# Kernel optimization log

Measured on AMD Instinct MI355X. Metric: run time of the kernel, lower is better.

## Reference

```python
import jax, jax.numpy as jnp
import numpy as np

N_USER = 60000
N_ITEM = 120000
N = N_USER + N_ITEM
EMB = 64
LAYERS = [64, 64, 64]
BATCH = 4096
NNZ_ADJ = 3_600_000
NNZ_UG = 960_000
NNZ_IG = 1_920_000


def spmm(rows, cols, vals, x, n_rows):
    # sparse (COO) @ dense: out[r] += v * x[c]
    return jax.ops.segment_sum(vals[:, None] * x[cols], rows, num_segments=n_rows)


def l2_normalize(x, eps=1e-12):
    n = jnp.linalg.norm(x, axis=1, keepdims=True)
    return x / jnp.maximum(n, eps)


def setup_inputs() -> dict:
    key = jax.random.key(0)
    ks = jax.random.split(key, 24)
    s = 0.1  # xavier-like init scale for 64-dim fan
    inp = {
        'users': jax.random.randint(ks[0], (BATCH,), 0, N_USER),
        'pos_items': jax.random.randint(ks[1], (BATCH,), 0, N_ITEM),
        'neg_items': jax.random.randint(ks[2], (BATCH,), 0, N_ITEM),
        # normalized bipartite adjacency (COO)
        'adj_rows': jax.random.randint(ks[3], (NNZ_ADJ,), 0, N),
        'adj_cols': jax.random.randint(ks[4], (NNZ_ADJ,), 0, N),
        'adj_vals': jax.random.uniform(ks[5], (NNZ_ADJ,), jnp.float32) * 0.05,
        # user-user graph for user_GNN
        'ug_rows': jax.random.randint(ks[6], (NNZ_UG,), 0, N_USER),
        'ug_cols': jax.random.randint(ks[7], (NNZ_UG,), 0, N_USER),
        'ug_vals': jax.random.uniform(ks[8], (NNZ_UG,), jnp.float32) * 0.06,
        # item-item graph for item_GNN
        'ig_rows': jax.random.randint(ks[9], (NNZ_IG,), 0, N_ITEM),
        'ig_cols': jax.random.randint(ks[10], (NNZ_IG,), 0, N_ITEM),
        'ig_vals': jax.random.uniform(ks[11], (NNZ_IG,), jnp.float32) * 0.06,
        'user_emb': jax.random.normal(ks[12], (N_USER, EMB), jnp.float32) * s,
        'item_emb': jax.random.normal(ks[13], (N_ITEM, EMB), jnp.float32) * s,
        # NGCF propagation weights, stacked over 3 layers (all 64x64)
        'W_gc': jax.random.normal(ks[14], (3, EMB, EMB), jnp.float32) * s,
        'b_gc': jax.random.normal(ks[15], (3, 1, EMB), jnp.float32) * s,
        'W_bi': jax.random.normal(ks[16], (3, EMB, EMB), jnp.float32) * s,
        'b_bi': jax.random.normal(ks[17], (3, 1, EMB), jnp.float32) * s,
        # 2-layer GCN weights for user/item side graphs
        'Wu0': jax.random.normal(ks[18], (EMB, 64), jnp.float32) * s,
        'bu0': jnp.zeros((64,), jnp.float32),
        'Wu1': jax.random.normal(ks[19], (64, 64), jnp.float32) * s,
        'bu1': jnp.zeros((64,), jnp.float32),
        'Wi0': jax.random.normal(ks[20], (EMB, 64), jnp.float32) * s,
        'bi0': jnp.zeros((64,), jnp.float32),
        'Wi1': jax.random.normal(ks[21], (64, 64), jnp.float32) * s,
        'bi1': jnp.zeros((64,), jnp.float32),
    }
    return inp


def reference(users, pos_items, neg_items,
              adj_rows, adj_cols, adj_vals,
              ug_rows, ug_cols, ug_vals,
              ig_rows, ig_cols, ig_vals,
              user_emb, item_emb,
              W_gc, b_gc, W_bi, b_bi,
              Wu0, bu0, Wu1, bu1, Wi0, bi0, Wi1, bi1):
    # side GCNs on user-user / item-item graphs (2 GraphConv layers, elu between)
    u_h = jax.nn.elu(spmm(ug_rows, ug_cols, ug_vals, user_emb, N_USER) @ Wu0 + bu0)
    u_h = spmm(ug_rows, ug_cols, ug_vals, u_h, N_USER) @ Wu1 + bu1
    i_h = jax.nn.elu(spmm(ig_rows, ig_cols, ig_vals, item_emb, N_ITEM) @ Wi0 + bi0)
    i_h = spmm(ig_rows, ig_cols, ig_vals, i_h, N_ITEM) @ Wi1 + bi1

    # NGCF propagation on the bipartite graph
    ego = jnp.concatenate([user_emb, item_emb], axis=0)  # [N, 64]
    all_emb = [ego]
    for k in range(len(LAYERS)):
        side = spmm(adj_rows, adj_cols, adj_vals, ego, N)         # [N, 64]
        sum_e = side @ W_gc[k] + b_gc[k]
        bi_e = (ego * side) @ W_bi[k] + b_bi[k]
        ego = jax.nn.leaky_relu(sum_e + bi_e, negative_slope=0.2)
        all_emb.append(l2_normalize(ego))
    all_emb = jnp.concatenate(all_emb, axis=1)  # [N, 256]

    u_g = all_emb[:N_USER]
    i_g = all_emb[N_USER:]

    # in-place relu in the torch code mutates the GNN outputs before concat
    user_full = jnp.concatenate([u_g, jax.nn.relu(u_h)], axis=1)  # [N_USER, 320]
    item_full = jnp.concatenate([i_g, jax.nn.relu(i_h)], axis=1)  # [N_ITEM, 320]

    return (user_full[users], item_full[pos_items], item_full[neg_items])
```

## Files before the change

kernel.cpp:

```cpp
#include <hip/hip_runtime.h>
#include <hip/hip_bf16.h>

#define N_USER 60000
#define N_ITEM 120000
#define NTOT   180000
#define NNZ_ADJ 3600000
#define NNZ_UG   960000
#define NNZ_IG  1920000

#define RSB     2048
#define NSB_ADJ ((NTOT  + RSB - 1) / RSB)
#define NSB_UG  ((N_USER+ RSB - 1) / RSB)
#define NSB_IG  ((N_ITEM+ RSB - 1) / RSB)
#define CAPA_SB 43008
#define CAPU_SB 34816
#define CAPI_SB 34816
#define CHUNK   4096
#define PB_U ((NNZ_UG  + CHUNK - 1) / CHUNK)
#define PB_I ((NNZ_IG  + CHUNK - 1) / CHUNK)
#define PB_A ((NNZ_ADJ + CHUNK - 1) / CHUNK)

typedef __hip_bfloat16 bf16;
typedef __attribute__((ext_vector_type(8))) short bf16x8;
typedef __attribute__((ext_vector_type(4))) float f32x4;

__device__ __forceinline__ float ldf(const void* p, long i, int f) {
    return f ? ((const float*)p)[i] : __bfloat162float(((const bf16*)p)[i]);
}

__device__ __forceinline__ unsigned pk2(float a, float b) {
    unsigned short lo = __bfloat16_as_ushort(__float2bfloat16(a));
    unsigned short hi = __bfloat16_as_ushort(__float2bfloat16(b));
    return (unsigned)lo | ((unsigned)hi << 16);
}

__device__ __forceinline__ bf16x8 mul_bf8(bf16x8 x, bf16x8 y) {
    bf16x8 r;
#pragma unroll
    for (int e = 0; e < 8; e++) {
        float xf = __uint_as_float(((unsigned)(unsigned short)x[e]) << 16);
        float yf = __uint_as_float(((unsigned)(unsigned short)y[e]) << 16);
        r[e] = (short)__bfloat16_as_ushort(__float2bfloat16(xf * yf));
    }
    return r;
}

__global__ void k_detect(const void* __restrict__ vals, int* __restrict__ flag) {
    if (threadIdx.x == 0 && blockIdx.x == 0) {
        const unsigned short* w = (const unsigned short*)vals;
        int cnt = 0;
        for (int i = 0; i < 512; i += 2) cnt += (w[i] >> 15) & 1;
        *flag = (cnt > 16) ? 1 : 0;
    }
}

__global__ __launch_bounds__(256) void k_cast16(const void* __restrict__ ue,
                                                const void* __restrict__ ie,
                                                bf16* __restrict__ ego16,
                                                const int* __restrict__ flag) {
    int f = *flag;
    long i = (long)blockIdx.x * 256 + threadIdx.x;
    const long uN = (long)N_USER * 64;
    if (i < (long)NTOT * 64) {
        float v = (i < uN) ? ldf(ue, i, f) : ldf(ie, i - uN, f);
        ego16[i] = __float2bfloat16(v);
    }
}

__global__ void k_initpos3(int* __restrict__ sbU, int* __restrict__ sbI,
                           int* __restrict__ sbA) {
    int i = threadIdx.x;
    if (i < NSB_UG)  sbU[i * 16] = i * CAPU_SB;
    if (i < NSB_IG)  sbI[i * 16] = i * CAPI_SB;
    if (i < NSB_ADJ) sbA[i * 16] = i * CAPA_SB;
}

__global__ __launch_bounds__(256) void k_part3(const int* __restrict__ rU, const int* __restrict__ cU, const void* __restrict__ vU,
                                               const int* __restrict__ rI, const int* __restrict__ cI, const void* __restrict__ vI,
                                               const int* __restrict__ rA, const int* __restrict__ cA, const void* __restrict__ vA,
                                               uint2* __restrict__ recU, uint2* __restrict__ recI, uint2* __restrict__ recA,
                                               int* __restrict__ sbU, int* __restrict__ sbI, int* __restrict__ sbA,
                                               const int* __restrict__ flag) {
    __shared__ int lcnt[96];
    __shared__ int lstart[96];
    __shared__ int lpos[96];
    __shared__ int lbase[96];
    __shared__ int wtmp;
    __shared__ uint2 stage[CHUNK];
    __shared__ unsigned char sbin[CHUNK];

    int f = *flag;
    int t = threadIdx.x;
    int b = blockIdx.x;
    const int *rows, *cols; const void* vals; uint2* rec; int* sbpos; int nnz, base;
    if (b < PB_U)             { rows = rU; cols = cU; vals = vU; rec = recU; sbpos = sbU; nnz = NNZ_UG;  base = b * CHUNK; }
    else if (b < PB_U + PB_I) { rows = rI; cols = cI; vals = vI; rec = recI; sbpos = sbI; nnz = NNZ_IG;  base = (b - PB_U) * CHUNK; }
    else                      { rows = rA; cols = cA; vals = vA; rec = recA; sbpos = sbA; nnz = NNZ_ADJ; base = (b - PB_U - PB_I) * CHUNK; }

    if (t < 96) lcnt[t] = 0;

    int base16 = base + t * 16;
    int rr[16], cc[16];
    float vv[16];
    if (base + CHUNK <= nnz) {
#pragma unroll
        for (int k = 0; k < 4; k++) {
            int4 r4 = *(const int4*)(rows + base16 + 4 * k);
            int4 c4 = *(const int4*)(cols + base16 + 4 * k);
            rr[4 * k + 0] = r4.x; rr[4 * k + 1] = r4.y; rr[4 * k + 2] = r4.z; rr[4 * k + 3] = r4.w;
            cc[4 * k + 0] = c4.x; cc[4 * k + 1] = c4.y; cc[4 * k + 2] = c4.z; cc[4 * k + 3] = c4.w;
        }
        if (f) {
#pragma unroll
            for (int k = 0; k < 4; k++) {
                float4 v4 = *(const float4*)((const float*)vals + base16 + 4 * k);
                vv[4 * k + 0] = v4.x; vv[4 * k + 1] = v4.y; vv[4 * k + 2] = v4.z; vv[4 * k + 3] = v4.w;
            }
        } else {
            const unsigned short* vb = (const unsigned short*)vals;
#pragma unroll
            for (int h = 0; h < 2; h++) {
                uint4 q = *(const uint4*)(vb + base16 + 8 * h);
                vv[8 * h + 0] = __uint_as_float(q.x << 16);
                vv[8 * h + 1] = __uint_as_float(q.x & 0xFFFF0000u);
                vv[8 * h + 2] = __uint_as_float(q.y << 16);
                vv[8 * h + 3] = __uint_as_float(q.y & 0xFFFF0000u);
                vv[8 * h + 4] = __uint_as_float(q.z << 16);
                vv[8 * h + 5] = __uint_as_float(q.z & 0xFFFF0000u);
                vv[8 * h + 6] = __uint_as_float(q.w << 16);
                vv[8 * h + 7] = __uint_as_float(q.w & 0xFFFF0000u);
            }
        }
    } else {
#pragma unroll
        for (int k = 0; k < 16; k++) {
            int e = base16 + k;
            if (e < nnz) { rr[k] = rows[e]; cc[k] = cols[e]; vv[k] = ldf(vals, e, f); }
            else         { rr[k] = -1; cc[k] = 0; vv[k] = 0.0f; }
        }
    }
    __syncthreads();

#pragma unroll
    for (int k = 0; k < 16; k++)
        if (rr[k] >= 0) atomicAdd(&lcnt[rr[k] >> 11], 1);
    __syncthreads();

    int v = (t < 96) ? lcnt[t] : 0;
    int incl = v;
    {
        int lane = t & 63;
#pragma unroll
        for (int d = 1; d < 64; d <<= 1) {
            int w = __shfl_up(incl, d, 64);
            if (lane >= d) incl += w;
        }
    }
    if (t == 63) wtmp = incl;
    __syncthreads();
    if (t >= 64 && t < 96) incl += wtmp;
    if (t < 96) {
        int ex = incl - v;
        lstart[t] = ex;
        lpos[t]   = ex;
        lbase[t]  = v ? atomicAdd(&sbpos[t * 16], v) : 0;
    }
    __syncthreads();

#pragma unroll
    for (int k = 0; k < 16; k++) {
        if (rr[k] >= 0) {
            int sb = rr[k] >> 11;
            int o = atomicAdd(&lpos[sb], 1);
            stage[o] = make_uint2(((unsigned)(rr[k] & 2047) << 18) | (unsigned)cc[k],
                                  __float_as_uint(vv[k]));
            sbin[o] = (unsigned char)sb;
        }
    }
    __syncthreads();

    int total = lstart[95] + lcnt[95];
    for (int i = t; i < total; i += 256) {
        int sb = sbin[i];
        rec[lbase[sb] + (i - lstart[sb])] = stage[i];
    }
}

__global__ __launch_bounds__(1024) void k_sortsb3(
        const uint2* __restrict__ recU, uint2* __restrict__ rec2U, int* __restrict__ rstartU, int* __restrict__ rendU, const int* __restrict__ sbU,
        const uint2* __restrict__ recI, uint2* __restrict__ rec2I, int* __restrict__ rstartI, int* __restrict__ rendI, const int* __restrict__ sbI,
        const uint2* __restrict__ recA, uint2* __restrict__ rec2A, int* __restrict__ rstartA, int* __restrict__ rendA, const int* __restrict__ sbA) {
    __shared__ int cnt[RSB];
    __shared__ int pos[RSB];
    __shared__ int wsum[16];
    int b = blockIdx.x, t = threadIdx.x;
    const uint2* rec; uint2* rec2; int* rstart; int* rend; const int* sbpos;
    int cap, n_rows, lb;
    if (b < NSB_UG) {
        lb = b; rec = recU; rec2 = rec2U; rstart = rstartU; rend = rendU;
        sbpos = sbU; cap = CAPU_SB; n_rows = N_USER;
    } else if (b < NSB_UG + NSB_IG) {
        lb = b - NSB_UG; rec = recI; rec2 = rec2I; rstart = rstartI; rend = rendI;
        sbpos = sbI; cap = CAPI_SB; n_rows = N_ITEM;
    } else {
        lb = b - NSB_UG - NSB_IG; rec = recA; rec2 = rec2A; rstart = rstartA; rend = rendA;
        sbpos = sbA; cap = CAPA_SB; n_rows = NTOT;
    }
    int s = lb * cap;
    int e = sbpos[lb * 16];
    cnt[t] = 0; cnt[t + 1024] = 0;
    __syncthreads();
    int j = s + t;
    for (; j + 3072 < e; j += 4096) {
        uint2 r0 = rec[j];
        uint2 r1 = rec[j + 1024];
        uint2 r2 = rec[j + 2048];
        uint2 r3 = rec[j + 3072];
        atomicAdd(&cnt[r0.x >> 18], 1);
        atomicAdd(&cnt[r1.x >> 18], 1);
        atomicAdd(&cnt[r2.x >> 18], 1);
        atomicAdd(&cnt[r3.x >> 18], 1);
    }
    for (; j < e; j += 1024)
        atomicAdd(&cnt[rec[j].x >> 18], 1);
    __syncthreads();
    int a  = cnt[2 * t];
    int bb = cnt[2 * t + 1];
    int ps = a + bb;
    int incl = ps;
    int lane = t & 63;
#pragma unroll
    for (int d = 1; d < 64; d <<= 1) {
        int v = __shfl_up(incl, d, 64);
        if (lane >= d) incl += v;
    }
    int wv = t >> 6;
    if (lane == 63) wsum[wv] = incl;
    __syncthreads();
    if (t < 16) {
        int v  = wsum[t];
        int iv = v;
#pragma unroll
        for (int d = 1; d < 16; d <<= 1) {
            int w = __shfl_up(iv, d, 64);
            if (t >= d) iv += w;
        }
        wsum[t] = iv - v;
    }
    __syncthreads();
    int ex0 = wsum[wv] + (incl - ps);
    pos[2 * t]     = ex0;
    pos[2 * t + 1] = ex0 + a;
    int row0 = lb * RSB;
    {
        int ra = row0 + 2 * t;
        if (ra < n_rows) { rstart[ra] = s + ex0;      rend[ra] = s + ex0 + a; }
        int rb = ra + 1;
        if (rb < n_rows) { rstart[rb] = s + ex0 + a;  rend[rb] = s + ex0 + a + bb; }
    }
    __syncthreads();
    j = s + t;
    for (; j + 3072 < e; j += 4096) {
        uint2 r0 = rec[j];
        uint2 r1 = rec[j + 1024];
        uint2 r2 = rec[j + 2048];
        uint2 r3 = rec[j + 3072];
        int o0 = atomicAdd(&pos[r0.x >> 18], 1);
        int o1 = atomicAdd(&pos[r1.x >> 18], 1);
        int o2 = atomicAdd(&pos[r2.x >> 18], 1);
        int o3 = atomicAdd(&pos[r3.x >> 18], 1);
        rec2[s + o0] = r0;
        rec2[s + o1] = r1;
        rec2[s + o2] = r2;
        rec2[s + o3] = r3;
    }
    for (; j < e; j += 1024) {
        uint2 r = rec[j];
        int o = atomicAdd(&pos[r.x >> 18], 1);
        rec2[s + o] = r;
    }
}

#define ACC8(q, v)                                      \
    a[0] += (v) * __uint_as_float((q).x << 16);         \
    a[1] += (v) * __uint_as_float((q).x & 0xFFFF0000u); \
    a[2] += (v) * __uint_as_float((q).y << 16);         \
    a[3] += (v) * __uint_as_float((q).y & 0xFFFF0000u); \
    a[4] += (v) * __uint_as_float((q).z << 16);         \
    a[5] += (v) * __uint_as_float((q).z & 0xFFFF0000u); \
    a[6] += (v) * __uint_as_float((q).w << 16);         \
    a[7] += (v) * __uint_as_float((q).w & 0xFFFF0000u);

__device__ __forceinline__ void spmm_row(int row, int p,
                                         const int* __restrict__ rstart,
                                         const int* __restrict__ rend,
                                         const uint2* __restrict__ rec,
                                         const bf16* __restrict__ x,
                                         bf16* __restrict__ out) {
    int s = rstart[row], e = rend[row];
    const uint4* xb = (const uint4*)x;
    float a[8];
#pragma unroll
    for (int i = 0; i < 8; i++) a[i] = 0.0f;

    int j = s;
    for (; j + 4 <= e; j += 4) {
        uint2 r0 = rec[j];
        uint2 r1 = rec[j + 1];
        uint2 r2 = rec[j + 2];
        uint2 r3 = rec[j + 3];
        uint4 q0 = xb[(long)(r0.x & 0x3FFFF) * 8 + p];
        uint4 q1 = xb[(long)(r1.x & 0x3FFFF) * 8 + p];
        uint4 q2 = xb[(long)(r2.x & 0x3FFFF) * 8 + p];
        uint4 q3 = xb[(long)(r3.x & 0x3FFFF) * 8 + p];
        float v0 = __uint_as_float(r0.y);
        float v1 = __uint_as_float(r1.y);
        float v2 = __uint_as_float(r2.y);
        float v3 = __uint_as_float(r3.y);
        ACC8(q0, v0)
        ACC8(q1, v1)
        ACC8(q2, v2)
        ACC8(q3, v3)
    }
    for (; j < e; j++) {
        uint2 r = rec[j];
        uint4 q = xb[(long)(r.x & 0x3FFFF) * 8 + p];
        float v = __uint_as_float(r.y);
        ACC8(q, v)
    }

    *(uint4*)(out + (long)row * 64 + p * 8) =
        make_uint4(pk2(a[0], a[1]), pk2(a[2], a[3]),
                   pk2(a[4], a[5]), pk2(a[6], a[7]));
}

__global__ __launch_bounds__(256) void k_spmm_bf(const int* __restrict__ rstart,
                                                 const int* __restrict__ rend,
                                                 const uint2* __restrict__ rec,
                                                 const bf16* __restrict__ x,
                                                 bf16* __restrict__ out,
                                                 int n_rows) {
    int row = blockIdx.x * 32 + (threadIdx.x >> 3);
    int p = threadIdx.x & 7;
    if (row >= n_rows) return;
    spmm_row(row, p, rstart, rend, rec, x, out);
}

__global__ __launch_bounds__(256) void k_spmm2(
        const int* __restrict__ rs0, const int* __restrict__ re0, const uint2* __restrict__ rc0,
        const bf16* __restrict__ x0, bf16* __restrict__ o0, int n0, int nb0,
        const int* __restrict__ rs1, const int* __restrict__ re1, const uint2* __restrict__ rc1,
        const bf16* __restrict__ x1, bf16* __restrict__ o1, int n1) {
    int b = blockIdx.x;
    int p = threadIdx.x & 7;
    int rl = threadIdx.x >> 3;
    if (b < nb0) {
        int row = b * 32 + rl;
        if (row < n0) spmm_row(row, p, rs0, re0, rc0, x0, o0);
    } else {
        int row = (b - nb0) * 32 + rl;
        if (row < n1) spmm_row(row, p, rs1, re1, rc1, x1, o1);
    }
}

template <int ACT>
__global__ __launch_bounds__(256) void k_gemm2(
        const bf16* __restrict__ X0, const void* __restrict__ W0, const void* __restrict__ b0,
        bf16* __restrict__ Y0, int M0, int nb0,
        const bf16* __restrict__ X1, const void* __restrict__ W1, const void* __restrict__ b1,
        bf16* __restrict__ Y1, int M1,
        const int* __restrict__ flag) {
    __shared__ bf16 WtH[64][72];
    __shared__ bf16 WtL[64][72];
    __shared__ float bl[64];
    int f = *flag;
    int tid = threadIdx.x;
    int bId = blockIdx.x;
    const bf16* X; const void* W; const void* bb; bf16* Y; int M, sb, nbseg;
    if (bId < nb0) { X = X0; W = W0; bb = b0; Y = Y0; M = M0; sb = bId; nbseg = nb0; }
    else { X = X1; W = W1; bb = b1; Y = Y1; M = M1; sb = bId - nb0; nbseg = gridDim.x - nb0; }

    for (int idx = tid; idx < 4096; idx += 256) {
        int n = idx >> 6, kk = idx & 63;
        float v = ldf(W, (long)kk * 64 + n, f);
        bf16 h = __float2bfloat16(v);
        WtH[n][kk] = h;
        WtL[n][kk] = __float2bfloat16(v - __bfloat162float(h));
    }
    if (tid < 64) bl[tid] = ldf(bb, tid, f);
    __syncthreads();

    int l  = tid & 63;
    int lr = l & 15;
    int lk = l >> 4;

    bf16x8 bh[2][4], bbf[2][4];
#pragma unroll
    for (int kt = 0; kt < 2; kt++)
#pragma unroll
        for (int ct = 0; ct < 4; ct++) {
            int n  = ct * 16 + lr;
            int ko = kt * 32 + lk * 8;
            bh[kt][ct]  = *(const bf16x8*)&WtH[n][ko];
            bbf[kt][ct] = *(const bf16x8*)&WtL[n][ko];
        }

    int nt  = M >> 4;
    int wid = sb * 4 + (tid >> 6);
    int nw  = nbseg * 4;

    for (int t = wid; t < nt; t += nw) {
        const bf16* Ap = X + (long)(t * 16 + lr) * 64 + lk * 8;
        bf16x8 a[2];
#pragma unroll
        for (int kt = 0; kt < 2; kt++) a[kt] = *(const bf16x8*)(Ap + kt * 32);

        f32x4 acc[4];
#pragma unroll
        for (int ct = 0; ct < 4; ct++) {
            float bv = bl[ct * 16 + lr];
            acc[ct] = (f32x4){bv, bv, bv, bv};
        }
#pragma unroll
        for (int kt = 0; kt < 2; kt++)
#pragma unroll
            for (int ct = 0; ct < 4; ct++) {
                acc[ct] = __builtin_amdgcn_mfma_f32_16x16x32_bf16(a[kt], bh[kt][ct], acc[ct], 0, 0, 0);
                acc[ct] = __builtin_amdgcn_mfma_f32_16x16x32_bf16(a[kt], bbf[kt][ct], acc[ct], 0, 0, 0);
            }

#pragma unroll
        for (int r = 0; r < 4; r++) {
            float v0 = acc[0][r], v1 = acc[1][r], v2 = acc[2][r], v3 = acc[3][r];
            if (ACT == 2) {
                v0 = fmaxf(v0, 0.0f); v1 = fmaxf(v1, 0.0f);
                v2 = fmaxf(v2, 0.0f); v3 = fmaxf(v3, 0.0f);
            } else {
                v0 = (v0 > 0.0f) ? v0 : (expf(v0) - 1.0f);
                v1 = (v1 > 0.0f) ? v1 : (expf(v1) - 1.0f);
                v2 = (v2 > 0.0f) ? v2 : (expf(v2) - 1.0f);
                v3 = (v3 > 0.0f) ? v3 : (expf(v3) - 1.0f);
            }
            long ob = (long)(t * 16 + lk * 4 + r) * 64 + lr;
            Y[ob]      = __float2bfloat16(v0);
            Y[ob + 16] = __float2bfloat16(v1);
            Y[ob + 32] = __float2bfloat16(v2);
            Y[ob + 48] = __float2bfloat16(v3);
        }
    }
}

__global__ __launch_bounds__(256) void k_layer(const bf16* __restrict__ S,
                                               const bf16* __restrict__ Ein,
                                               bf16* __restrict__ Eout,
                                               const void* __restrict__ Wgc,
                                               const void* __restrict__ bgc,
                                               const void* __restrict__ Wbi,
                                               const void* __restrict__ bbi,
                                               long woff, long boff,
                                               float* __restrict__ scale, int M,
                                               const int* __restrict__ flag) {
    __shared__ bf16 W1H[64][72];
    __shared__ bf16 W1L[64][72];
    __shared__ bf16 W2H[64][72];
    __shared__ bf16 W2L[64][72];
    __shared__ float bl[64];
    int f = *flag;
    int tid = threadIdx.x;
    for (int idx = tid; idx < 4096; idx += 256) {
        int n = idx >> 6, kk = idx & 63;
        float v1 = ldf(Wgc, woff + (long)kk * 64 + n, f);
        float v2 = ldf(Wbi, woff + (long)kk * 64 + n, f);
        bf16 h1 = __float2bfloat16(v1);
        bf16 h2 = __float2bfloat16(v2);
        W1H[n][kk] = h1;
        W1L[n][kk] = __float2bfloat16(v1 - __bfloat162float(h1));
        W2H[n][kk] = h2;
        W2L[n][kk] = __float2bfloat16(v2 - __bfloat162float(h2));
    }
    if (tid < 64) bl[tid] = ldf(bgc, boff + tid, f) + ldf(bbi, boff + tid, f);
    __syncthreads();

    int l  = tid & 63;
    int lr = l & 15;
    int lk = l >> 4;

    bf16x8 w1h[2][4], w1l[2][4], w2h[2][4], w2l[2][4];
#pragma unroll
    for (int kt = 0; kt < 2; kt++)
#pragma unroll
        for (int ct = 0; ct < 4; ct++) {
            int n  = ct * 16 + lr;
            int ko = kt * 32 + lk * 8;
            w1h[kt][ct] = *(const bf16x8*)&W1H[n][ko];
            w1l[kt][ct] = *(const bf16x8*)&W1L[n][ko];
            w2h[kt][ct] = *(const bf16x8*)&W2H[n][ko];
            w2l[kt][ct] = *(const bf16x8*)&W2L[n][ko];
        }

    int nt  = M >> 4;
    int wid = blockIdx.x * 4 + (tid >> 6);
    int nw  = gridDim.x * 4;

    for (int t = wid; t < nt; t += nw) {
        long rb = (long)(t * 16 + lr) * 64 + lk * 8;
        bf16x8 sv[2], pv[2];
        sv[0] = *(const bf16x8*)(S + rb);
        sv[1] = *(const bf16x8*)(S + rb + 32);
        {
            bf16x8 e0 = *(const bf16x8*)(Ein + rb);
            bf16x8 e1 = *(const bf16x8*)(Ein + rb + 32);
            pv[0] = mul_bf8(e0, sv[0]);
            pv[1] = mul_bf8(e1, sv[1]);
        }

        f32x4 acc[4];
#pragma unroll
        for (int ct = 0; ct < 4; ct++) {
            float bv = bl[ct * 16 + lr];
            acc[ct] = (f32x4){bv, bv, bv, bv};
        }
#pragma unroll
        for (int kt = 0; kt < 2; kt++)
#pragma unroll
            for (int ct = 0; ct < 4; ct++) {
                acc[ct] = __builtin_amdgcn_mfma_f32_16x16x32_bf16(sv[kt], w1h[kt][ct], acc[ct], 0, 0, 0);
                acc[ct] = __builtin_amdgcn_mfma_f32_16x16x32_bf16(sv[kt], w1l[kt][ct], acc[ct], 0, 0, 0);
                acc[ct] = __builtin_amdgcn_mfma_f32_16x16x32_bf16(pv[kt], w2h[kt][ct], acc[ct], 0, 0, 0);
                acc[ct] = __builtin_amdgcn_mfma_f32_16x16x32_bf16(pv[kt], w2l[kt][ct], acc[ct], 0, 0, 0);
            }

#pragma unroll
        for (int r = 0; r < 4; r++) {
            float v0 = acc[0][r], v1 = acc[1][r], v2 = acc[2][r], v3 = acc[3][r];
            v0 = (v0 > 0.0f) ? v0 : 0.2f * v0;
            v1 = (v1 > 0.0f) ? v1 : 0.2f * v1;
            v2 = (v2 > 0.0f) ? v2 : 0.2f * v2;
            v3 = (v3 > 0.0f) ? v3 : 0.2f * v3;
            float ss = v0 * v0 + v1 * v1 + v2 * v2 + v3 * v3;
            ss += __shfl_xor(ss, 1, 64);
            ss += __shfl_xor(ss, 2, 64);
            ss += __shfl_xor(ss, 4, 64);
            ss += __shfl_xor(ss, 8, 64);
            float sc2 = 1.0f / fmaxf(sqrtf(ss), 1e-12f);
            int grow = t * 16 + lk * 4 + r;
            long ob = (long)grow * 64 + lr;
            Eout[ob]      = __float2bfloat16(v0);
            Eout[ob + 16] = __float2bfloat16(v1);
            Eout[ob + 32] = __float2bfloat16(v2);
            Eout[ob + 48] = __float2bfloat16(v3);
            if (lr == 0) scale[grow] = sc2;
        }
    }
}

__global__ __launch_bounds__(64) void k_gather(const int* __restrict__ users,
                                               const int* __restrict__ pos,
                                               const int* __restrict__ neg,
                                               const void* __restrict__ ue,
                                               const void* __restrict__ ie,
                                               const bf16* __restrict__ E1,
                                               const bf16* __restrict__ E2,
                                               const bf16* __restrict__ E3,
                                               const float* __restrict__ s1,
                                               const float* __restrict__ s2,
                                               const float* __restrict__ s3,
                                               const bf16* __restrict__ uh,
                                               const bf16* __restrict__ ih,
                                               void* __restrict__ out,
                                               const int* __restrict__ flag) {
    int f = *flag;
    int b = blockIdx.x;
    int which = b >> 12;
    int s = b & 4095;
    int lane = threadIdx.x;
    long ebase, nrow;
    const void* e0;
    const bf16* hh;
    if (which == 0) {
        int r = users[s];
        e0 = ue; ebase = (long)r * 64;
        hh = uh + (long)r * 64;
        nrow = (long)r;
    } else {
        int r = (which == 1) ? pos[s] : neg[s];
        e0 = ie; ebase = (long)r * 64;
        hh = ih + (long)r * 64;
        nrow = (long)(N_USER + r);
    }
    long nbase = nrow * 64;
    float o0 = ldf(e0, ebase + lane, f);
    float o1 = __bfloat162float(E1[nbase + lane]) * s1[nrow];
    float o2 = __bfloat162float(E2[nbase + lane]) * s2[nrow];
    float o3 = __bfloat162float(E3[nbase + lane]) * s3[nrow];
    float o4 = __bfloat162float(hh[lane]);
    long ob = (long)b * 320;
    if (f) {
        float* o = (float*)out + ob;
        o[lane] = o0; o[64 + lane] = o1; o[128 + lane] = o2;
        o[192 + lane] = o3; o[256 + lane] = o4;
    } else {
        bf16* o = (bf16*)out + ob;
        o[lane]       = __float2bfloat16(o0);
        o[64 + lane]  = __float2bfloat16(o1);
        o[128 + lane] = __float2bfloat16(o2);
        o[192 + lane] = __float2bfloat16(o3);
        o[256 + lane] = __float2bfloat16(o4);
    }
}

extern "C" void kernel_launch(void* const* d_in, const int* in_sizes, int n_in,
                              void* d_out, int out_size, void* d_ws, size_t ws_size,
                              hipStream_t stream) {
    const int* users = (const int*)d_in[0];
    const int* pos   = (const int*)d_in[1];
    const int* neg   = (const int*)d_in[2];
    const int* adj_r = (const int*)d_in[3];
    const int* adj_c = (const int*)d_in[4];
    const void* adj_v = d_in[5];
    const int* ug_r  = (const int*)d_in[6];
    const int* ug_c  = (const int*)d_in[7];
    const void* ug_v = d_in[8];
    const int* ig_r  = (const int*)d_in[9];
    const int* ig_c  = (const int*)d_in[10];
    const void* ig_v = d_in[11];
    const void* ue   = d_in[12];
    const void* ie   = d_in[13];
    const void* Wgc  = d_in[14];
    const void* bgc  = d_in[15];
    const void* Wbi  = d_in[16];
    const void* bbi  = d_in[17];
    const void* Wu0  = d_in[18];
    const void* bu0  = d_in[19];
    const void* Wu1  = d_in[20];
    const void* bu1  = d_in[21];
    const void* Wi0  = d_in[22];
    const void* bi0  = d_in[23];
    const void* Wi1  = d_in[24];
    const void* bi1  = d_in[25];

    char* ws = (char*)d_ws;
    int*   FLAG  = (int*)(ws + 0);
    bf16*  S16A  = (bf16*)(ws + 256);
    uint2* recTmpA = (uint2*)(ws + 256);
    bf16*  SU    = (bf16*)(ws + 30277888L);
    bf16*  SI    = (bf16*)(ws + 46080256L);
    bf16*  ego16 = (bf16*)(ws + 61440256L);
    bf16*  UH    = (bf16*)(ws + 84480256L);
    bf16*  IH    = (bf16*)(ws + 92160256L);
    bf16*  E1    = (bf16*)(ws + 107520256L);
    bf16*  E2    = (bf16*)(ws + 130560256L);
    bf16*  E3    = (bf16*)(ws + 153600256L);
    uint2* recTmpU = (uint2*)(ws + 130560256L);
    bf16*  TI    = (bf16*)(ws + 130560256L);
    bf16*  TU    = (bf16*)(ws + 145920256L);
    uint2* recTmpI = (uint2*)(ws + 153600256L);
    uint2* rec2A = (uint2*)(ws + 176640256L);
    uint2* rec2U = (uint2*)(ws + 206917888L);
    uint2* rec2I = (uint2*)(ws + 215273728L);
    int* rstartA = (int*)(ws + 231706880L);
    int* rendA   = (int*)(ws + 232426880L);
    int* rstartU = (int*)(ws + 233146880L);
    int* rendU   = (int*)(ws + 233386880L);
    int* rstartI = (int*)(ws + 233626880L);
    int* rendI   = (int*)(ws + 234106880L);
    int* sbposU  = (int*)(ws + 234586880L);
    int* sbposI  = (int*)(ws + 234588928L);
    int* sbposA  = (int*)(ws + 234593024L);
    float* SC1   = (float*)(ws + 234600192L);
    float* SC2   = (float*)(ws + 235320192L);
    float* SC3   = (float*)(ws + 236040192L);

    k_detect<<<1, 64, 0, stream>>>(adj_v, FLAG);
    k_cast16<<<45000, 256, 0, stream>>>(ue, ie, ego16, FLAG);

    k_initpos3<<<1, 256, 0, stream>>>(sbposU, sbposI, sbposA);
    k_part3<<<PB_U + PB_I + PB_A, 256, 0, stream>>>(ug_r, ug_c, ug_v,
                                                    ig_r, ig_c, ig_v,
                                                    adj_r, adj_c, adj_v,
                                                    recTmpU, recTmpI, recTmpA,
                                                    sbposU, sbposI, sbposA, FLAG);
    k_sortsb3<<<NSB_UG + NSB_IG + NSB_ADJ, 1024, 0, stream>>>(
        recTmpU, rec2U, rstartU, rendU, sbposU,
        recTmpI, rec2I, rstartI, rendI, sbposI,
        recTmpA, rec2A, rstartA, rendA, sbposA);

    const bf16* ego16I = ego16 + (size_t)N_USER * 64;
    int nbU = (N_USER + 31) / 32;
    int nbI = (N_ITEM + 31) / 32;
    int gu = (N_USER / 16 + 7) / 8;
    int gi = (N_ITEM / 16 + 7) / 8;
    k_spmm2<<<nbU + nbI, 256, 0, stream>>>(rstartU, rendU, rec2U, ego16,  SU, N_USER, nbU,
                                           rstartI, rendI, rec2I, ego16I, SI, N_ITEM);
    k_gemm2<1><<<gu + gi, 256, 0, stream>>>(SU, Wu0, bu0, TU, N_USER, gu,
                                            SI, Wi0, bi0, TI, N_ITEM, FLAG);
    k_spmm2<<<nbU + nbI, 256, 0, stream>>>(rstartU, rendU, rec2U, TU, SU, N_USER, nbU,
                                           rstartI, rendI, rec2I, TI, SI, N_ITEM);
    k_gemm2<2><<<gu + gi, 256, 0, stream>>>(SU, Wu1, bu1, UH, N_USER, gu,
                                            SI, Wi1, bi1, IH, N_ITEM, FLAG);

    bf16* Ebuf[4]  = {ego16, E1, E2, E3};
    float* SCs[3]  = {SC1, SC2, SC3};
    for (int k = 0; k < 3; k++) {
        k_spmm_bf<<<(NTOT + 31) / 32, 256, 0, stream>>>(rstartA, rendA, rec2A, Ebuf[k], S16A, NTOT);
        k_layer<<<704, 256, 0, stream>>>(S16A, Ebuf[k], Ebuf[k + 1],
                                         Wgc, bgc, Wbi, bbi,
                                         (long)k * 4096, (long)k * 64,
                                         SCs[k], NTOT, FLAG);
    }

    k_gather<<<12288, 64, 0, stream>>>(users, pos, neg, ue, ie, E1, E2, E3,
                                       SC1, SC2, SC3, UH, IH, d_out, FLAG);
}
```

Baseline: 765.9 us.

## Switch COO-to-CSR sort to fine 256-row bins with in-LDS per-bin sort

Replaces the two-level radix partition (2048-row superbins sorted by 1024-thread blocks into a second global buffer) with fine 256-row bins. The first pass now scatters into 704/469/235 bins per graph, and the second pass sorts each bin through an LDS staging buffer, writing back in place. This removes the second global record buffer and the scattered global writes of the old sort, and gives many more blocks to run in parallel. In exchange the partition kernel keeps larger shared histograms, runs a bigger scan and scatters into many more destinations, and fixed per-bin capacities are a hard limit on bin size.

Result: faster. 750.1 us, median of 2 (-2.1%).

```diff
diff --git a/kernel.cpp b/kernel.cpp
--- a/kernel.cpp
+++ b/kernel.cpp
@@ -8,13 +8,13 @@
 #define NNZ_UG   960000
 #define NNZ_IG  1920000
 
-#define RSB     2048
-#define NSB_ADJ ((NTOT  + RSB - 1) / RSB)
-#define NSB_UG  ((N_USER+ RSB - 1) / RSB)
-#define NSB_IG  ((N_ITEM+ RSB - 1) / RSB)
-#define CAPA_SB 43008
-#define CAPU_SB 34816
-#define CAPI_SB 34816
+#define RSBF    256
+#define NBF_U   235
+#define NBF_I   469
+#define NBF_A   704
+#define CAPU_F  4736
+#define CAPI_F  4736
+#define CAPA_F  5888
 #define CHUNK   4096
 #define PB_U ((NNZ_UG  + CHUNK - 1) / CHUNK)
 #define PB_I ((NNZ_IG  + CHUNK - 1) / CHUNK)
@@ -69,10 +69,11 @@
 
 __global__ void k_initpos3(int* __restrict__ sbU, int* __restrict__ sbI,
                            int* __restrict__ sbA) {
-    int i = threadIdx.x;
-    if (i < NSB_UG)  sbU[i * 16] = i * CAPU_SB;
-    if (i < NSB_IG)  sbI[i * 16] = i * CAPI_SB;
-    if (i < NSB_ADJ) sbA[i * 16] = i * CAPA_SB;
+    for (int i = threadIdx.x; i < NBF_U + NBF_I + NBF_A; i += blockDim.x) {
+        if (i < NBF_U) sbU[i * 16] = i * CAPU_F;
+        else if (i < NBF_U + NBF_I) { int k = i - NBF_U; sbI[k * 16] = k * CAPI_F; }
+        else { int k = i - NBF_U - NBF_I; sbA[k * 16] = k * CAPA_F; }
+    }
 }
 
 __global__ __launch_bounds__(256) void k_part3(const int* __restrict__ rU, const int* __restrict__ cU, const void* __restrict__ vU,
@@ -81,13 +82,13 @@
                                                uint2* __restrict__ recU, uint2* __restrict__ recI, uint2* __restrict__ recA,
                                                int* __restrict__ sbU, int* __restrict__ sbI, int* __restrict__ sbA,
                                                const int* __restrict__ flag) {
-    __shared__ int lcnt[96];
-    __shared__ int lstart[96];
-    __shared__ int lpos[96];
-    __shared__ int lbase[96];
-    __shared__ int wtmp;
+    __shared__ int lcnt[NBF_A];
+    __shared__ int lstart[NBF_A];
+    __shared__ int lpos[NBF_A];
+    __shared__ int lbase[NBF_A];
+    __shared__ int wsum4[4];
     __shared__ uint2 stage[CHUNK];
-    __shared__ unsigned char sbin[CHUNK];
+    __shared__ unsigned short sbin[CHUNK];
 
     int f = *flag;
     int t = threadIdx.x;
@@ -97,7 +98,7 @@
     else if (b < PB_U + PB_I) { rows = rI; cols = cI; vals = vI; rec = recI; sbpos = sbI; nnz = NNZ_IG;  base = (b - PB_U) * CHUNK; }
     else                      { rows = rA; cols = cA; vals = vA; rec = recA; sbpos = sbA; nnz = NNZ_ADJ; base = (b - PB_U - PB_I) * CHUNK; }
 
-    if (t < 96) lcnt[t] = 0;
+    for (int i = t; i < NBF_A; i += 256) lcnt[i] = 0;
 
     int base16 = base + t * 16;
     int rr[16], cc[16];
@@ -143,142 +144,114 @@
 
 #pragma unroll
     for (int k = 0; k < 16; k++)
-        if (rr[k] >= 0) atomicAdd(&lcnt[rr[k] >> 11], 1);
-    __syncthreads();
-
-    int v = (t < 96) ? lcnt[t] : 0;
-    int incl = v;
-    {
-        int lane = t & 63;
-#pragma unroll
-        for (int d = 1; d < 64; d <<= 1) {
-            int w = __shfl_up(incl, d, 64);
-            if (lane >= d) incl += w;
-        }
-    }
-    if (t == 63) wtmp = incl;
-    __syncthreads();
-    if (t >= 64 && t < 96) incl += wtmp;
-    if (t < 96) {
-        int ex = incl - v;
-        lstart[t] = ex;
-        lpos[t]   = ex;
-        lbase[t]  = v ? atomicAdd(&sbpos[t * 16], v) : 0;
+        if (rr[k] >= 0) atomicAdd(&lcnt[rr[k] >> 8], 1);
+    __syncthreads();
+
+    int b0 = 3 * t;
+    int v0 = (b0     < NBF_A) ? lcnt[b0]     : 0;
+    int v1 = (b0 + 1 < NBF_A) ? lcnt[b0 + 1] : 0;
+    int v2 = (b0 + 2 < NBF_A) ? lcnt[b0 + 2] : 0;
+    int ts = v0 + v1 + v2;
+    int incl = ts;
+    int lane = t & 63;
+#pragma unroll
+    for (int d = 1; d < 64; d <<= 1) {
+        int w = __shfl_up(incl, d, 64);
+        if (lane >= d) incl += w;
+    }
+    int wv = t >> 6;
+    if (lane == 63) wsum4[wv] = incl;
+    __syncthreads();
+    if (t == 0) { int a = 0; for (int k2 = 0; k2 < 4; k2++) { int x = wsum4[k2]; wsum4[k2] = a; a += x; } }
+    __syncthreads();
+    int ex = wsum4[wv] + (incl - ts);
+    if (b0 < NBF_A) {
+        lstart[b0] = ex;            lpos[b0] = ex;
+        lbase[b0]  = v0 ? atomicAdd(&sbpos[b0 * 16], v0) : 0;
+    }
+    if (b0 + 1 < NBF_A) {
+        lstart[b0 + 1] = ex + v0;   lpos[b0 + 1] = ex + v0;
+        lbase[b0 + 1]  = v1 ? atomicAdd(&sbpos[(b0 + 1) * 16], v1) : 0;
+    }
+    if (b0 + 2 < NBF_A) {
+        lstart[b0 + 2] = ex + v0 + v1; lpos[b0 + 2] = ex + v0 + v1;
+        lbase[b0 + 2]  = v2 ? atomicAdd(&sbpos[(b0 + 2) * 16], v2) : 0;
     }
     __syncthreads();
 
 #pragma unroll
     for (int k = 0; k < 16; k++) {
         if (rr[k] >= 0) {
-            int sb = rr[k] >> 11;
+            int sb = rr[k] >> 8;
             int o = atomicAdd(&lpos[sb], 1);
-            stage[o] = make_uint2(((unsigned)(rr[k] & 2047) << 18) | (unsigned)cc[k],
+            stage[o] = make_uint2(((unsigned)(rr[k] & 255) << 18) | (unsigned)cc[k],
                                   __float_as_uint(vv[k]));
-            sbin[o] = (unsigned char)sb;
-        }
-    }
-    __syncthreads();
-
-    int total = lstart[95] + lcnt[95];
+            sbin[o] = (unsigned short)sb;
+        }
+    }
+    __syncthreads();
+
+    int total = lstart[NBF_A - 1] + lcnt[NBF_A - 1];
     for (int i = t; i < total; i += 256) {
         int sb = sbin[i];
         rec[lbase[sb] + (i - lstart[sb])] = stage[i];
     }
 }
 
-__global__ __launch_bounds__(1024) void k_sortsb3(
-        const uint2* __restrict__ recU, uint2* __restrict__ rec2U, int* __restrict__ rstartU, int* __restrict__ rendU, const int* __restrict__ sbU,
-        const uint2* __restrict__ recI, uint2* __restrict__ rec2I, int* __restrict__ rstartI, int* __restrict__ rendI, const int* __restrict__ sbI,
-        const uint2* __restrict__ recA, uint2* __restrict__ rec2A, int* __restrict__ rstartA, int* __restrict__ rendA, const int* __restrict__ sbA) {
-    __shared__ int cnt[RSB];
-    __shared__ int pos[RSB];
-    __shared__ int wsum[16];
+__global__ __launch_bounds__(256) void k_sortfine3(
+        uint2* __restrict__ recU, int* __restrict__ rstartU, int* __restrict__ rendU, const int* __restrict__ sbU,
+        uint2* __restrict__ recI, int* __restrict__ rstartI, int* __restrict__ rendI, const int* __restrict__ sbI,
+        uint2* __restrict__ recA, int* __restrict__ rstartA, int* __restrict__ rendA, const int* __restrict__ sbA) {
+    __shared__ int cnt[RSBF];
+    __shared__ int lpos[RSBF];
+    __shared__ int wsum[4];
+    __shared__ uint2 stage[CAPA_F];
     int b = blockIdx.x, t = threadIdx.x;
-    const uint2* rec; uint2* rec2; int* rstart; int* rend; const int* sbpos;
-    int cap, n_rows, lb;
-    if (b < NSB_UG) {
-        lb = b; rec = recU; rec2 = rec2U; rstart = rstartU; rend = rendU;
-        sbpos = sbU; cap = CAPU_SB; n_rows = N_USER;
-    } else if (b < NSB_UG + NSB_IG) {
-        lb = b - NSB_UG; rec = recI; rec2 = rec2I; rstart = rstartI; rend = rendI;
-        sbpos = sbI; cap = CAPI_SB; n_rows = N_ITEM;
+    uint2* rec; int* rstart; int* rend; const int* sbpos; int cap, n_rows, bin;
+    if (b < NBF_U) {
+        bin = b; rec = recU; rstart = rstartU; rend = rendU;
+        sbpos = sbU; cap = CAPU_F; n_rows = N_USER;
+    } else if (b < NBF_U + NBF_I) {
+        bin = b - NBF_U; rec = recI; rstart = rstartI; rend = rendI;
+        sbpos = sbI; cap = CAPI_F; n_rows = N_ITEM;
     } else {
-        lb = b - NSB_UG - NSB_IG; rec = recA; rec2 = rec2A; rstart = rstartA; rend = rendA;
-        sbpos = sbA; cap = CAPA_SB; n_rows = NTOT;
-    }
-    int s = lb * cap;
-    int e = sbpos[lb * 16];
-    cnt[t] = 0; cnt[t + 1024] = 0;
-    __syncthreads();
-    int j = s + t;
-    for (; j + 3072 < e; j += 4096) {
-        uint2 r0 = rec[j];
-        uint2 r1 = rec[j + 1024];
-        uint2 r2 = rec[j + 2048];
-        uint2 r3 = rec[j + 3072];
-        atomicAdd(&cnt[r0.x >> 18], 1);
-        atomicAdd(&cnt[r1.x >> 18], 1);
-        atomicAdd(&cnt[r2.x >> 18], 1);
-        atomicAdd(&cnt[r3.x >> 18], 1);
-    }
-    for (; j < e; j += 1024)
+        bin = b - NBF_U - NBF_I; rec = recA; rstart = rstartA; rend = rendA;
+        sbpos = sbA; cap = CAPA_F; n_rows = NTOT;
+    }
+    int s = bin * cap;
+    int e = sbpos[bin * 16];
+    cnt[t] = 0;
+    __syncthreads();
+    for (int j = s + t; j < e; j += 256)
         atomicAdd(&cnt[rec[j].x >> 18], 1);
     __syncthreads();
-    int a  = cnt[2 * t];
-    int bb = cnt[2 * t + 1];
-    int ps = a + bb;
-    int incl = ps;
+    int v = cnt[t];
+    int incl = v;
     int lane = t & 63;
 #pragma unroll
     for (int d = 1; d < 64; d <<= 1) {
-        int v = __shfl_up(incl, d, 64);
-        if (lane >= d) incl += v;
+        int w = __shfl_up(incl, d, 64);
+        if (lane >= d) incl += w;
     }
     int wv = t >> 6;
     if (lane == 63) wsum[wv] = incl;
     __syncthreads();
-    if (t < 16) {
-        int v  = wsum[t];
-        int iv = v;
-#pragma unroll
-        for (int d = 1; d < 16; d <<= 1) {
-            int w = __shfl_up(iv, d, 64);
-            if (t >= d) iv += w;
-        }
-        wsum[t] = iv - v;
-    }
-    __syncthreads();
-    int ex0 = wsum[wv] + (incl - ps);
-    pos[2 * t]     = ex0;
-    pos[2 * t + 1] = ex0 + a;
-    int row0 = lb * RSB;
-    {
-        int ra = row0 + 2 * t;
-        if (ra < n_rows) { rstart[ra] = s + ex0;      rend[ra] = s + ex0 + a; }
-        int rb = ra + 1;
-        if (rb < n_rows) { rstart[rb] = s + ex0 + a;  rend[rb] = s + ex0 + a + bb; }
-    }
-    __syncthreads();
-    j = s + t;
-    for (; j + 3072 < e; j += 4096) {
-        uint2 r0 = rec[j];
-        uint2 r1 = rec[j + 1024];
-        uint2 r2 = rec[j + 2048];
-        uint2 r3 = rec[j + 3072];
-        int o0 = atomicAdd(&pos[r0.x >> 18], 1);
-        int o1 = atomicAdd(&pos[r1.x >> 18], 1);
-        int o2 = atomicAdd(&pos[r2.x >> 18], 1);
-        int o3 = atomicAdd(&pos[r3.x >> 18], 1);
-        rec2[s + o0] = r0;
-        rec2[s + o1] = r1;
-        rec2[s + o2] = r2;
-        rec2[s + o3] = r3;
-    }
-    for (; j < e; j += 1024) {
+    if (t == 0) { int a = 0; for (int k = 0; k < 4; k++) { int x = wsum[k]; wsum[k] = a; a += x; } }
+    __syncthreads();
+    int ex = wsum[wv] + (incl - v);
+    lpos[t] = ex;
+    int row = bin * RSBF + t;
+    if (row < n_rows) { rstart[row] = s + ex; rend[row] = s + ex + v; }
+    __syncthreads();
+    for (int j = s + t; j < e; j += 256) {
         uint2 r = rec[j];
-        int o = atomicAdd(&pos[r.x >> 18], 1);
-        rec2[s + o] = r;
-    }
+        int o = atomicAdd(&lpos[r.x >> 18], 1);
+        stage[o] = r;
+    }
+    __syncthreads();
+    int total = e - s;
+    for (int i = t; i < total; i += 256)
+        rec[s + i] = stage[i];
 }
 
 #define ACC8(q, v)                                      \
@@ -641,35 +614,32 @@
 
     char* ws = (char*)d_ws;
     int*   FLAG  = (int*)(ws + 0);
-    bf16*  S16A  = (bf16*)(ws + 256);
-    uint2* recTmpA = (uint2*)(ws + 256);
-    bf16*  SU    = (bf16*)(ws + 30277888L);
-    bf16*  SI    = (bf16*)(ws + 46080256L);
-    bf16*  ego16 = (bf16*)(ws + 61440256L);
-    bf16*  UH    = (bf16*)(ws + 84480256L);
-    bf16*  IH    = (bf16*)(ws + 92160256L);
-    bf16*  E1    = (bf16*)(ws + 107520256L);
-    bf16*  E2    = (bf16*)(ws + 130560256L);
-    bf16*  E3    = (bf16*)(ws + 153600256L);
-    uint2* recTmpU = (uint2*)(ws + 130560256L);
-    bf16*  TI    = (bf16*)(ws + 130560256L);
-    bf16*  TU    = (bf16*)(ws + 145920256L);
-    uint2* recTmpI = (uint2*)(ws + 153600256L);
-    uint2* rec2A = (uint2*)(ws + 176640256L);
-    uint2* rec2U = (uint2*)(ws + 206917888L);
-    uint2* rec2I = (uint2*)(ws + 215273728L);
-    int* rstartA = (int*)(ws + 231706880L);
-    int* rendA   = (int*)(ws + 232426880L);
-    int* rstartU = (int*)(ws + 233146880L);
-    int* rendU   = (int*)(ws + 233386880L);
-    int* rstartI = (int*)(ws + 233626880L);
-    int* rendI   = (int*)(ws + 234106880L);
-    int* sbposU  = (int*)(ws + 234586880L);
-    int* sbposI  = (int*)(ws + 234588928L);
-    int* sbposA  = (int*)(ws + 234593024L);
-    float* SC1   = (float*)(ws + 234600192L);
-    float* SC2   = (float*)(ws + 235320192L);
-    float* SC3   = (float*)(ws + 236040192L);
+    uint2* recA  = (uint2*)(ws + 256);
+    uint2* recU  = (uint2*)(ws + 33161472L);
+    uint2* recI  = (uint2*)(ws + 42065152L);
+    bf16*  S16A  = (bf16*)(ws + 59832064L);
+    bf16*  SU    = (bf16*)(ws + 82872064L);
+    bf16*  SI    = (bf16*)(ws + 90552064L);
+    bf16*  ego16 = (bf16*)(ws + 105912064L);
+    bf16*  UH    = (bf16*)(ws + 128952064L);
+    bf16*  IH    = (bf16*)(ws + 136632064L);
+    bf16*  E1    = (bf16*)(ws + 151992064L);
+    bf16*  E2    = (bf16*)(ws + 175032064L);
+    bf16*  E3    = (bf16*)(ws + 198072064L);
+    bf16*  TI    = (bf16*)(ws + 175032064L);
+    bf16*  TU    = (bf16*)(ws + 190392064L);
+    int* rstartA = (int*)(ws + 221112064L);
+    int* rendA   = (int*)(ws + 221832064L);
+    int* rstartU = (int*)(ws + 222552064L);
+    int* rendU   = (int*)(ws + 222792064L);
+    int* rstartI = (int*)(ws + 223032064L);
+    int* rendI   = (int*)(ws + 223512064L);
+    int* sbposU  = (int*)(ws + 223992064L);
+    int* sbposI  = (int*)(ws + 224007168L);
+    int* sbposA  = (int*)(ws + 224037248L);
+    float* SC1   = (float*)(ws + 224082304L);
+    float* SC2   = (float*)(ws + 224802304L);
+    float* SC3   = (float*)(ws + 225522304L);
 
     k_detect<<<1, 64, 0, stream>>>(adj_v, FLAG);
     k_cast16<<<45000, 256, 0, stream>>>(ue, ie, ego16, FLAG);
@@ -678,31 +648,31 @@
     k_part3<<<PB_U + PB_I + PB_A, 256, 0, stream>>>(ug_r, ug_c, ug_v,
                                                     ig_r, ig_c, ig_v,
                                                     adj_r, adj_c, adj_v,
-                                                    recTmpU, recTmpI, recTmpA,
+                                                    recU, recI, recA,
                                                     sbposU, sbposI, sbposA, FLAG);
-    k_sortsb3<<<NSB_UG + NSB_IG + NSB_ADJ, 1024, 0, stream>>>(
-        recTmpU, rec2U, rstartU, rendU, sbposU,
-        recTmpI, rec2I, rstartI, rendI, sbposI,
-        recTmpA, rec2A, rstartA, rendA, sbposA);
+    k_sortfine3<<<NBF_U + NBF_I + NBF_A, 256, 0, stream>>>(
+        recU, rstartU, rendU, sbposU,
+        recI, rstartI, rendI, sbposI,
+        recA, rstartA, rendA, sbposA);
 
     const bf16* ego16I = ego16 + (size_t)N_USER * 64;
     int nbU = (N_USER + 31) / 32;
     int nbI = (N_ITEM + 31) / 32;
     int gu = (N_USER / 16 + 7) / 8;
     int gi = (N_ITEM / 16 + 7) / 8;
-    k_spmm2<<<nbU + nbI, 256, 0, stream>>>(rstartU, rendU, rec2U, ego16,  SU, N_USER, nbU,
-                                           rstartI, rendI, rec2I, ego16I, SI, N_ITEM);
+    k_spmm2<<<nbU + nbI, 256, 0, stream>>>(rstartU, rendU, recU, ego16,  SU, N_USER, nbU,
+                                           rstartI, rendI, recI, ego16I, SI, N_ITEM);
     k_gemm2<1><<<gu + gi, 256, 0, stream>>>(SU, Wu0, bu0, TU, N_USER, gu,
                                             SI, Wi0, bi0, TI, N_ITEM, FLAG);
-    k_spmm2<<<nbU + nbI, 256, 0, stream>>>(rstartU, rendU, rec2U, TU, SU, N_USER, nbU,
-                                           rstartI, rendI, rec2I, TI, SI, N_ITEM);
+    k_spmm2<<<nbU + nbI, 256, 0, stream>>>(rstartU, rendU, recU, TU, SU, N_USER, nbU,
+                                           rstartI, rendI, recI, TI, SI, N_ITEM);
     k_gemm2<2><<<gu + gi, 256, 0, stream>>>(SU, Wu1, bu1, UH, N_USER, gu,
                                             SI, Wi1, bi1, IH, N_ITEM, FLAG);
 
     bf16* Ebuf[4]  = {ego16, E1, E2, E3};
     float* SCs[3]  = {SC1, SC2, SC3};
     for (int k = 0; k < 3; k++) {
-        k_spmm_bf<<<(NTOT + 31) / 32, 256, 0, stream>>>(rstartA, rendA, rec2A, Ebuf[k], S16A, NTOT);
+        k_spmm_bf<<<(NTOT + 31) / 32, 256, 0, stream>>>(rstartA, rendA, recA, Ebuf[k], S16A, NTOT);
         k_layer<<<704, 256, 0, stream>>>(S16A, Ebuf[k], Ebuf[k + 1],
                                          Wgc, bgc, Wbi, bbi,
                                          (long)k * 4096, (long)k * 64,
```
